# Optimization experiments

Hardware: AMD Instinct MI355X
Metric: run time of the kernel (lower is better)

Reference implementation:

```python
import jax, jax.numpy as jnp
from jax import lax
import numpy as np

# ---- init hyperparameters (from init_kwargs) ----
STRIDE = 1
DP_CHANNELS = 1
ATOM_R = 8
ATOM_C = 8
NUMB_ATOM = 128
T_SC = 3
K = 256
BATCH = 32
IMG = 64


def setup_inputs() -> dict:
    key = jax.random.key(0)
    k1, k2 = jax.random.split(key)
    Y = jax.random.normal(k1, (BATCH, DP_CHANNELS, IMG, IMG), dtype=jnp.float32)
    # ConvTranspose2d weight layout: (numb_atom, dp_channels, atom_c, atom_r)
    W = jax.random.normal(k2, (NUMB_ATOM, DP_CHANNELS, ATOM_C, ATOM_R), dtype=jnp.float32)
    # normalise_weights(): each (i, j) filter divided by its L2 norm
    W = W / jnp.sqrt(jnp.sum(W ** 2, axis=(2, 3), keepdims=True))
    return {"Y": Y, "W_D": W}


def _conv_D(X, W):
    # PyTorch ConvTranspose2d (stride=1, no padding): full convolution with
    # spatially-flipped kernel; W is (in=numb_atom, out=dp_channels, kh, kw).
    kh, kw = W.shape[2], W.shape[3]
    return lax.conv_general_dilated(
        X, jnp.flip(W, (2, 3)), (1, 1),
        [(kh - 1, kh - 1), (kw - 1, kw - 1)],
        dimension_numbers=('NCHW', 'IOHW', 'NCHW'))


def _conv_Dt(R, Wt):
    # PyTorch Conv2d (VALID, stride=1): Wt is (out=numb_atom, in=dp, kh, kw)
    return lax.conv_general_dilated(
        R, Wt, (1, 1), 'VALID', dimension_numbers=('NCHW', 'OIHW', 'NCHW'))


def _hard_threshold_k(X, k):
    # keep the k largest-|.| entries per sample (over flattened C,H,W)
    B = X.shape[0]
    flat = X.reshape(B, -1)
    _, idx = lax.top_k(jnp.abs(flat), k)                      # [B, k]
    vals = jnp.take_along_axis(flat, idx, axis=1)             # [B, k]
    out = jnp.zeros_like(flat).at[jnp.arange(B)[:, None], idx].set(vals)
    return out.reshape(X.shape)


def _linesearch(Y, X, W, Wt, k):
    R = Y - _conv_D(X, W)
    g = _conv_Dt(R, Wt)
    l2_start = jnp.sum(R ** 2)

    def attempt(alpha):
        Xu = _hard_threshold_k(X + alpha * g, k)
        err = jnp.sum((Y - _conv_D(Xu, W)) ** 2)
        return Xu, err

    Xu0, err0 = attempt(jnp.float32(1.0))

    def cond(s):
        _, _, err, count = s
        return (err >= l2_start) & (count <= 15)

    def body(s):
        alpha, _, _, count = s
        alpha = alpha * jnp.float32(0.5)
        Xu, err = attempt(alpha)
        return (alpha, Xu, err, count + 1)

    alpha, Xu, err, _ = lax.while_loop(
        cond, body, (jnp.float32(1.0), Xu0, err0, jnp.int32(0)))
    return Xu, err, alpha


def reference(Y, W_D):
    # D_trans.weight = D.weight.permute(0,1,3,2) -> (numb_atom, dp, atom_r, atom_c)
    Wt = jnp.swapaxes(W_D, 2, 3)
    kh, kw = Wt.shape[2], Wt.shape[3]
    B, _, H, W_sp = Y.shape
    X = jnp.zeros((B, W_D.shape[0], H - kh + 1, W_sp - kw + 1), dtype=Y.dtype)
    for _ in range(T_SC):
        X, _, _ = _linesearch(Y, X, W_D, Wt, K)
    return X
```

## Files before the change

### kernel.cpp

```cpp
#include <hip/hip_runtime.h>
#include <stdint.h>

#define NB   32
#define NCH  128
#define IMG  64
#define IMG2 4096
#define OH   57
#define OHW  3249
#define CHW  415872
#define KTOP 256
#define NATT 17
#define NS   32
#define SCAP 512
#define NCAP 1536
#define NBUCK 8192
#define HSHIFT 18
#define TGT  512
#define RSTRIDE 72
#define NZB  257
#define BMW  12996

typedef unsigned long long ull;

__global__ void k_init(int* support_cnt) {
    if (threadIdx.x < NB) support_cnt[threadIdx.x] = 0;
}

__global__ __launch_bounds__(256) void k_resid(
    const float* __restrict__ Y, const float* __restrict__ W,
    const double* __restrict__ l2prev, const double* __restrict__ errv,
    const uint32_t* __restrict__ sel_idx, const float* __restrict__ sel_val, int t,
    int* __restrict__ support_cnt, ull* __restrict__ sup_iv,
    float* __restrict__ Rg, double* __restrict__ l2cur,
    uint32_t* __restrict__ hist, int* __restrict__ zero_arena)
{
    int bx = blockIdx.x, tid = threadIdx.x;
    if (bx >= NB) {
        int zb = bx - NB;
        if (zb < 256) {
            ((uint4*)hist)[zb * 256 + tid] = make_uint4(0u, 0u, 0u, 0u);
        } else {
            ((uint4*)zero_arena)[tid] = make_uint4(0u, 0u, 0u, 0u);
            ((uint4*)zero_arena)[tid + 256] = make_uint4(0u, 0u, 0u, 0u);
        }
        return;
    }
    int b = bx;
    __shared__ float Rs[IMG2];
    __shared__ uint32_t s_si[KTOP];
    __shared__ float s_sv[KTOP];
    __shared__ double red[256];
    __shared__ int a_sh;

    const float4* Y4 = (const float4*)(Y + b * IMG2);
    float4* R4 = (float4*)Rs;
    for (int i = tid; i < IMG2 / 4; i += 256) R4[i] = Y4[i];

    int n = 0;
    if (t > 0) {
        if (tid < NATT) {
            double e = 0.0;
#pragma unroll 8
            for (int b2 = 0; b2 < NB; ++b2) e += errv[tid * NB + b2];
            red[tid] = e;
        } else if (tid == NATT) {
            double l2 = 0.0;
#pragma unroll 8
            for (int b2 = 0; b2 < NB; ++b2) l2 += l2prev[b2];
            red[NATT] = l2;
        }
        __syncthreads();
        if (tid == 0) {
            double l2 = red[NATT];
            int sel = NATT - 1;
            for (int a2 = 0; a2 < NATT; ++a2) if (red[a2] < l2) { sel = a2; break; }
            a_sh = sel;
        }
        __syncthreads();
        int a = a_sh;
        size_t o = ((size_t)a * NB + b) * KTOP;
        uint32_t mi = sel_idx[o + tid];
        float mv = sel_val[o + tid];
        s_si[tid] = mi;
        s_sv[tid] = mv;
        sup_iv[b * KTOP + tid] = (ull)mi | ((ull)__float_as_uint(mv) << 32);
        if (tid == 0) support_cnt[b] = KTOP;
        n = KTOP;
    }
    __syncthreads();

    for (int task = tid; task < n * 64; task += 256) {
        int i = task >> 6, tap = task & 63, p = tap >> 3, q = tap & 7;
        uint32_t idx = s_si[i];
        float val = s_sv[i];
        int c = idx / OHW, rem = idx % OHW, s = rem / OH, tt = rem % OH;
        float w = W[c * 64 + p * 8 + q];
        atomicAdd(&Rs[(s + p) * IMG + (tt + q)], -val * w);
    }
    __syncthreads();
    double acc = 0.0;
    for (int i = tid; i < IMG2; i += 256) {
        float v = Rs[i];
        Rg[b * IMG2 + i] = v;
        acc += (double)v * (double)v;
    }
    red[tid] = acc; __syncthreads();
    for (int s2 = 128; s2 > 0; s2 >>= 1) { if (tid < s2) red[tid] += red[tid + s2]; __syncthreads(); }
    if (tid == 0) l2cur[b] = red[0];
}

__global__ __launch_bounds__(256) void k_conv(
    const float* __restrict__ Rg, const float* __restrict__ W,
    float* __restrict__ g_out, uint32_t* __restrict__ hist,
    int* __restrict__ done_cnt, uint32_t* __restrict__ thr)
{
    int b = blockIdx.x, cg0 = blockIdx.y, tid = threadIdx.x;
    __shared__ float Rs[71 * 72];
    __shared__ uint32_t hl[NBUCK];
    __shared__ int elect_sh;
    for (int i = tid; i < 71 * 72; i += 256) Rs[i] = 0.f;
    for (int i = tid; i < NBUCK; i += 256) hl[i] = 0u;
    __syncthreads();
    const float4* R4 = (const float4*)(Rg + b * IMG2);
    for (int i = tid; i < 1024; i += 256) {
        int row = i >> 4, col4 = (i & 15) * 4;
        *(float4*)&Rs[row * 72 + col4] = R4[i];
    }
    __syncthreads();
    int csub = tid >> 7;
    int tile = tid & 127;
    bool active = tile < 120;
    int tr = active ? tile / 15 : 0;
    int tc = active ? tile % 15 : 0;
    int s0 = tr * 8, t0 = tc * 4;

    for (int sub = 0; sub < 4; ++sub) {
        int c = cg0 * 8 + sub * 2 + csub;
        int c_s = __builtin_amdgcn_readfirstlane(c);
        const float* Wc = W + c_s * 64;

        float acc[8][4];
#pragma unroll
        for (int r = 0; r < 8; ++r)
#pragma unroll
            for (int cc = 0; cc < 4; ++cc) acc[r][cc] = 0.f;

#pragma unroll
        for (int rho = 0; rho < 15; ++rho) {
            float rb[12];
            const float* rp = &Rs[(s0 + rho) * 72 + t0];
            *(float4*)&rb[0] = *(const float4*)rp;
            *(float4*)&rb[4] = *(const float4*)(rp + 4);
            *(float4*)&rb[8] = *(const float4*)(rp + 8);
#pragma unroll
            for (int r = 0; r < 8; ++r) {
                const int p = rho - r;
                if (p >= 0 && p < 8) {
#pragma unroll
                    for (int q = 0; q < 8; ++q) {
                        float wv = Wc[q * 8 + p];
#pragma unroll
                        for (int cc = 0; cc < 4; ++cc)
                            acc[r][cc] = fmaf(rb[cc + q], wv, acc[r][cc]);
                    }
                }
            }
        }
        if (active) {
            float* go = g_out + (size_t)(b * NCH + c) * OHW;
#pragma unroll
            for (int r = 0; r < 8; ++r) {
                int s = s0 + r;
                if (s < OH) {
#pragma unroll
                    for (int cc = 0; cc < 4; ++cc) {
                        int t = t0 + cc;
                        if (t < OH) {
                            float v = acc[r][cc];
                            go[s * OH + t] = v;
                            uint32_t bits = __float_as_uint(v) & 0x7fffffffu;
                            atomicAdd(&hl[bits >> HSHIFT], 1u);
                        }
                    }
                }
            }
        }
    }
    __syncthreads();
    for (int i = tid; i < NBUCK; i += 256) {
        uint32_t v = hl[i];
        if (v) atomicAdd(&hist[b * NBUCK + i], v);
    }
    __syncthreads();
    if (tid == 0) {
        __threadfence();
        int old = atomicAdd(&done_cnt[b], 1);
        elect_sh = (old == 15) ? 1 : 0;
    }
    __syncthreads();
    if (elect_sh) {
        uint32_t h[32];
        uint32_t s = 0;
        const uint32_t* hb = hist + b * NBUCK + tid * 32;
#pragma unroll
        for (int k = 0; k < 32; ++k) {
            h[k] = __hip_atomic_load(&hb[k], __ATOMIC_RELAXED, __HIP_MEMORY_SCOPE_AGENT);
            s += h[k];
        }
        uint32_t* buf0 = hl;
        uint32_t* buf1 = hl + 256;
        int cur = 0;
        buf0[tid] = s;
        __syncthreads();
        for (int d = 1; d < 256; d <<= 1) {
            uint32_t* bc = cur ? buf1 : buf0;
            uint32_t* bn = cur ? buf0 : buf1;
            uint32_t v = bc[tid];
            if (tid + d < 256) v += bc[tid + d];
            bn[tid] = v;
            cur ^= 1;
            __syncthreads();
        }
        uint32_t* bc = cur ? buf1 : buf0;
        uint32_t sufme = bc[tid];
        uint32_t base  = (tid < 255) ? bc[tid + 1] : 0u;
        if (tid == 0 && bc[0] < TGT) thr[b] = 0u;
        if (base < TGT && sufme >= TGT) {
            uint32_t acc2 = base; int bk = 0;
#pragma unroll
            for (int k = 31; k >= 0; --k) {
                acc2 += h[k];
                if (acc2 >= TGT) { bk = tid * 32 + k; break; }
            }
            thr[b] = (uint32_t)bk << HSHIFT;
        }
    }
}

__global__ __launch_bounds__(256) void k_collect(
    const float* __restrict__ g, const uint32_t* __restrict__ thr,
    int* __restrict__ cand_cnt, uint32_t* __restrict__ cand_idx, float* __restrict__ cand_g)
{
    int b = blockIdx.y;
    int i4 = blockIdx.x * 256 + threadIdx.x;
    if (i4 >= CHW / 4) return;
    int slice = blockIdx.x & (NS - 1);
    uint32_t tb = thr[b];
    float4 v4 = ((const float4*)(g + (size_t)b * CHW))[i4];
    float vv[4] = { v4.x, v4.y, v4.z, v4.w };
#pragma unroll
    for (int k = 0; k < 4; ++k) {
        uint32_t bits = __float_as_uint(vv[k]) & 0x7fffffffu;
        if (bits >= tb) {
            int pos = atomicAdd(&cand_cnt[b * NS + slice], 1);
            if (pos < SCAP) {
                cand_idx[(b * NS + slice) * SCAP + pos] = (uint32_t)(i4 * 4 + k);
                cand_g[(b * NS + slice) * SCAP + pos] = vv[k];
            }
        }
    }
}

__global__ __launch_bounds__(1024) void k_suppg(
    const float* __restrict__ g,
    const int* __restrict__ support_cnt, const ull* __restrict__ sup_iv,
    const int* __restrict__ cand_cnt, const uint32_t* __restrict__ cand_idx,
    const float* __restrict__ cand_g,
    uint4* __restrict__ ns_pack, ull* __restrict__ sup_gp, ull* __restrict__ kb_all)
{
    int b = blockIdx.x, tid = threadIdx.x, lane = tid & 63;
    __shared__ uint32_t bm[BMW];
    __shared__ int cnts[NS];
    __shared__ ull ck[NCAP];
    __shared__ float cg_l[NCAP];
    __shared__ int nns_sh;
    int n = support_cnt[b];
    for (int i = tid; i < BMW / 4; i += 1024) ((uint4*)bm)[i] = make_uint4(0u, 0u, 0u, 0u);
    if (tid < NS) cnts[tid] = min(cand_cnt[b * NS + tid], SCAP);
    if (tid == 0) nns_sh = 0;
    __syncthreads();
    if (tid < KTOP) {
        float gv = 0.f, vs = 0.f;
        uint32_t nidx;
        if (tid < n) {
            ull iv = sup_iv[b * KTOP + tid];
            uint32_t idx = (uint32_t)iv;
            nidx = idx;
            vs = __uint_as_float((uint32_t)(iv >> 32));
            atomicOr(&bm[idx >> 5], 1u << (idx & 31));
            gv = g[(size_t)b * CHW + idx];
            int c = idx / OHW, r = idx % OHW, s = r / OH, t = r % OH;
            uint32_t pk = (uint32_t)((c << 12) | (s << 6) | t);
            sup_gp[b * KTOP + tid] = ((ull)__float_as_uint(gv) << 32) | (ull)pk;
        } else {
            nidx = (uint32_t)(CHW + tid);
            sup_gp[b * KTOP + tid] = 0ull;
        }
        ull klo = (ull)(uint32_t)(~nidx);
#pragma unroll
        for (int a2 = 0; a2 < NATT; ++a2) {
            float v2 = (tid < n) ? fmaf(ldexpf(1.f, -a2), gv, vs) : 0.f;
            kb_all[((size_t)a2 * NB + b) * KTOP + tid] =
                ((ull)(__float_as_uint(v2) & 0x7fffffffu) << 32) | klo;
        }
    }
    __syncthreads();
    for (int t0 = tid; t0 < NS * SCAP; t0 += 1024) {
        int s = t0 >> 9, j = t0 & (SCAP - 1);
        bool keep = false; uint32_t idx = 0; float gv = 0.f;
        if (j < cnts[s]) {
            idx = cand_idx[(b * NS + s) * SCAP + j];
            gv = cand_g[(b * NS + s) * SCAP + j];
            keep = ((bm[idx >> 5] >> (idx & 31)) & 1u) == 0u;
        }
        ull mk = __ballot(keep);
        if (mk) {
            int basep = 0;
            if (lane == 0) basep = atomicAdd(&nns_sh, (int)__popcll(mk));
            basep = __shfl(basep, 0, 64);
            if (keep) {
                int p = basep + (int)__popcll(mk & ((1ull << lane) - 1ull));
                if (p < NCAP) {
                    ck[p] = ((ull)(__float_as_uint(gv) & 0x7fffffffu) << 32) | (ull)(uint32_t)(~idx);
                    cg_l[p] = gv;
                }
            }
        }
    }
    __syncthreads();
    int nns = min(nns_sh, NCAP);
    int nns8 = (nns + 7) & ~7;
    for (int i = nns + tid; i < nns8; i += 1024) ck[i] = 0ull;
    __syncthreads();
    ull myk[2]; int myr[2];
#pragma unroll
    for (int q = 0; q < 2; ++q) { int i = tid + 1024 * q; myk[q] = (i < nns) ? ck[i] : 0ull; myr[q] = 0; }
    for (int j = 0; j < nns8; j += 8) {
        ull t0 = ck[j], t1 = ck[j+1], t2 = ck[j+2], t3 = ck[j+3];
        ull t4 = ck[j+4], t5 = ck[j+5], t6 = ck[j+6], t7 = ck[j+7];
#pragma unroll
        for (int q = 0; q < 2; ++q) {
            myr[q] += ((t0 > myk[q]) ? 1 : 0) + ((t1 > myk[q]) ? 1 : 0)
                    + ((t2 > myk[q]) ? 1 : 0) + ((t3 > myk[q]) ? 1 : 0)
                    + ((t4 > myk[q]) ? 1 : 0) + ((t5 > myk[q]) ? 1 : 0)
                    + ((t6 > myk[q]) ? 1 : 0) + ((t7 > myk[q]) ? 1 : 0);
        }
    }
#pragma unroll
    for (int q = 0; q < 2; ++q) {
        int i = tid + 1024 * q;
        if (i < nns && myr[q] < KTOP) {
            uint32_t idx = ~(uint32_t)myk[q];
            int r = myr[q];
            int c = idx / OHW, rr = idx % OHW, s = rr / OH, t = rr % OH;
            uint32_t pk = (uint32_t)((c << 12) | (s << 6) | t);
            ns_pack[b * KTOP + r] = make_uint4(idx, __float_as_uint(cg_l[i]), pk, 0u);
        }
    }
}

__global__ __launch_bounds__(512) void k_att2(
    const float* __restrict__ Y, const float* __restrict__ W,
    const int* __restrict__ support_cnt, const ull* __restrict__ sup_iv,
    const ull* __restrict__ sup_gp, const uint4* __restrict__ ns_pack,
    const ull* __restrict__ kb_all,
    uint32_t* __restrict__ sel_idx, float* __restrict__ sel_val, double* __restrict__ err)
{
    int a = blockIdx.x, b = blockIdx.y, tid = threadIdx.x;
    int lane = tid & 63, wid = tid >> 6;
    float alpha = ldexpf(1.f, -a);
    int n = support_cnt[b];

    __shared__ float recon[64 * RSTRIDE];
    __shared__ ull kA[KTOP];
    __shared__ ull s_pv[KTOP];
    __shared__ uint32_t s_idx[KTOP];
    __shared__ double redd[8];

    uint32_t myi = 0, mypk = 0;
    float myv = 0.f;
    ull myk = 0;
    if (tid < KTOP) {
        uint4 np = ns_pack[b * KTOP + tid];
        myi = np.x;
        myv = alpha * __uint_as_float(np.y);
        mypk = np.z;
        myk = ((ull)(__float_as_uint(myv) & 0x7fffffffu) << 32) | (ull)(uint32_t)(~myi);
        kA[tid] = myk;
    } else {
        int t2 = tid - KTOP;
        ull gp = sup_gp[b * KTOP + t2];
        ull iv = sup_iv[b * KTOP + t2];
        if (t2 < n) {
            myi = (uint32_t)iv;
            myv = fmaf(alpha, __uint_as_float((uint32_t)(gp >> 32)),
                       __uint_as_float((uint32_t)(iv >> 32)));
            mypk = (uint32_t)gp;
        } else {
            myi = (uint32_t)(CHW + t2);
            myv = 0.f; mypk = 0u;
        }
        myk = ((ull)(__float_as_uint(myv) & 0x7fffffffu) << 32) | (ull)(uint32_t)(~myi);
    }

    const float4* Y4 = (const float4*)(Y + b * IMG2);
    float4 y0 = Y4[tid * 2], y1 = Y4[tid * 2 + 1];

    for (int i = tid; i < 64 * RSTRIDE; i += 512) recon[i] = 0.f;
    __syncthreads();

    const ull* __restrict__ kb = kb_all + ((size_t)a * NB + b) * KTOP;
    int cb0 = 0, cb1 = 0;
    for (int j = 0; j < KTOP; j += 8) {
        ull t0 = kb[j],     t1 = kb[j + 1], t2 = kb[j + 2], t3 = kb[j + 3];
        ull t4 = kb[j + 4], t5 = kb[j + 5], t6 = kb[j + 6], t7 = kb[j + 7];
        cb0 += ((t0 > myk) ? 1 : 0) + ((t1 > myk) ? 1 : 0)
             + ((t2 > myk) ? 1 : 0) + ((t3 > myk) ? 1 : 0);
        cb1 += ((t4 > myk) ? 1 : 0) + ((t5 > myk) ? 1 : 0)
             + ((t6 > myk) ? 1 : 0) + ((t7 > myk) ? 1 : 0);
    }
    int cb = cb0 + cb1;
    int rank;
    if (tid < KTOP) {
        rank = tid + cb;
    } else {
        int lo = 0, hi = KTOP;
        while (lo < hi) { int mid = (lo + hi) >> 1; if (kA[mid] > myk) lo = mid + 1; else hi = mid; }
        rank = lo + cb;
    }
    if (rank < KTOP) {
        s_pv[rank] = ((ull)__float_as_uint(myv) << 32) | (ull)mypk;
        s_idx[rank] = myi;
    }
    __syncthreads();

    {
        int p = lane >> 3, q = lane & 7;
        ull pv[4]; float wv[4];
#pragma unroll
        for (int j = 0; j < 4; ++j) pv[j] = s_pv[wid + 8 * j];
#pragma unroll
        for (int j = 0; j < 4; ++j) wv[j] = W[(((uint32_t)pv[j]) >> 12) * 64 + lane];
#pragma unroll
        for (int k4 = 0; k4 < 32; k4 += 4) {
            ull npv[4] = {0, 0, 0, 0}; float nwv[4] = {0.f, 0.f, 0.f, 0.f};
            if (k4 + 4 < 32) {
#pragma unroll
                for (int j = 0; j < 4; ++j) npv[j] = s_pv[wid + 8 * (k4 + 4 + j)];
#pragma unroll
                for (int j = 0; j < 4; ++j) nwv[j] = W[(((uint32_t)npv[j]) >> 12) * 64 + lane];
            }
#pragma unroll
            for (int j = 0; j < 4; ++j) {
                uint32_t pk = (uint32_t)pv[j];
                float val = __uint_as_float((uint32_t)(pv[j] >> 32));
                int s = (pk >> 6) & 63, t = pk & 63;
                atomicAdd(&recon[(s + p) * RSTRIDE + (t + q)], val * wv[j]);
            }
#pragma unroll
            for (int j = 0; j < 4; ++j) { pv[j] = npv[j]; wv[j] = nwv[j]; }
        }
    }
    __syncthreads();

    double accd = 0.0;
    {
        int idx0 = tid * 2;
        const float* rr = &recon[(idx0 >> 4) * RSTRIDE + (idx0 & 15) * 4];
        float d0 = y0.x - rr[0]; accd += (double)d0 * (double)d0;
        float d1 = y0.y - rr[1]; accd += (double)d1 * (double)d1;
        float d2 = y0.z - rr[2]; accd += (double)d2 * (double)d2;
        float d3 = y0.w - rr[3]; accd += (double)d3 * (double)d3;
        int idx1 = tid * 2 + 1;
        rr = &recon[(idx1 >> 4) * RSTRIDE + (idx1 & 15) * 4];
        float e0 = y1.x - rr[0]; accd += (double)e0 * (double)e0;
        float e1 = y1.y - rr[1]; accd += (double)e1 * (double)e1;
        float e2 = y1.z - rr[2]; accd += (double)e2 * (double)e2;
        float e3 = y1.w - rr[3]; accd += (double)e3 * (double)e3;
    }
    for (int d = 32; d > 0; d >>= 1) accd += __shfl_xor(accd, d, 64);
    if (lane == 0) redd[wid] = accd;
    __syncthreads();
    if (tid == 0) {
        double e = 0.0;
#pragma unroll
        for (int w2 = 0; w2 < 8; ++w2) e += redd[w2];
        err[a * NB + b] = e;
    }

    if (tid < KTOP) {
        size_t o = ((size_t)a * NB + b) * KTOP;
        ull pvt = s_pv[tid];
        sel_idx[o + tid] = s_idx[tid];
        sel_val[o + tid] = __uint_as_float((uint32_t)(pvt >> 32));
    }
}

__global__ void k_outzero(float4* __restrict__ out) {
    int i = blockIdx.x * 256 + threadIdx.x;
    if (i < (NB * CHW) / 4) out[i] = make_float4(0.f, 0.f, 0.f, 0.f);
}

__global__ __launch_bounds__(256) void k_scatter2(
    const double* __restrict__ l2f, const double* __restrict__ errv,
    const uint32_t* __restrict__ sel_idx, const float* __restrict__ sel_val,
    float* __restrict__ out)
{
    int b = blockIdx.x, tid = threadIdx.x;
    __shared__ double red2[NATT + 1];
    __shared__ int a_sh;
    if (tid < NATT) {
        double e = 0.0;
#pragma unroll 8
        for (int b2 = 0; b2 < NB; ++b2) e += errv[tid * NB + b2];
        red2[tid] = e;
    } else if (tid == NATT) {
        double l2 = 0.0;
#pragma unroll 8
        for (int b2 = 0; b2 < NB; ++b2) l2 += l2f[b2];
        red2[NATT] = l2;
    }
    __syncthreads();
    if (tid == 0) {
        double l2 = red2[NATT];
        int sel = NATT - 1;
        for (int a2 = 0; a2 < NATT; ++a2) if (red2[a2] < l2) { sel = a2; break; }
        a_sh = sel;
    }
    __syncthreads();
    size_t o = ((size_t)a_sh * NB + b) * KTOP;
    out[(size_t)b * CHW + sel_idx[o + tid]] = sel_val[o + tid];
}

static size_t align256(size_t x) { return (x + 255) & ~(size_t)255; }

extern "C" void kernel_launch(void* const* d_in, const int* in_sizes, int n_in,
                              void* d_out, int out_size, void* d_ws, size_t ws_size,
                              hipStream_t stream)
{
    const float* Y = (const float*)d_in[0];
    const float* W = (const float*)d_in[1];
    float* out = (float*)d_out;

    char* p = (char*)d_ws;
    size_t off = 0;
    auto carve = [&](size_t bytes) { void* r = p + off; off = align256(off + bytes); return r; };
    float*    Rg          = (float*)   carve(NB * IMG2 * sizeof(float));
    uint32_t* hist        = (uint32_t*)carve((size_t)NB * NBUCK * sizeof(uint32_t));
    uint32_t* thr         = (uint32_t*)carve(NB * sizeof(uint32_t));
    int*      zero_arena  = (int*)     carve(8192 * sizeof(int));
    double*   l2part      = (double*)  carve(2 * NB * sizeof(double));
    double*   err         = (double*)  carve((size_t)NATT * NB * sizeof(double));
    int*      support_cnt = (int*)     carve(NB * sizeof(int));
    ull*      sup_iv      = (ull*)     carve((size_t)NB * KTOP * sizeof(ull));
    uint32_t* sel_idx     = (uint32_t*)carve((size_t)NATT * NB * KTOP * sizeof(uint32_t));
    float*    sel_val     = (float*)   carve((size_t)NATT * NB * KTOP * sizeof(float));
    uint32_t* cand_idx    = (uint32_t*)carve((size_t)NB * NS * SCAP * sizeof(uint32_t));
    float*    cand_g      = (float*)   carve((size_t)NB * NS * SCAP * sizeof(float));
    uint4*    ns_pack     = (uint4*)   carve((size_t)NB * KTOP * sizeof(uint4));
    ull*      sup_gp      = (ull*)     carve((size_t)NB * KTOP * sizeof(ull));
    ull*      kb_all      = (ull*)     carve((size_t)NATT * NB * KTOP * sizeof(ull));
    (void)ws_size; (void)in_sizes; (void)n_in; (void)out_size;

    int*      cand_cnt    = zero_arena;
    int*      done_cnt    = zero_arena + 1024;

    k_init<<<1, 64, 0, stream>>>(support_cnt);
    for (int t = 0; t < 3; ++t) {
        double* l2cur  = l2part + (t & 1) * NB;
        double* l2prev = l2part + ((t + 1) & 1) * NB;
        k_resid<<<NB + NZB, 256, 0, stream>>>(Y, W, l2prev, err, sel_idx, sel_val, t,
                                              support_cnt, sup_iv, Rg, l2cur, hist, zero_arena);
        k_conv<<<dim3(NB, 16), 256, 0, stream>>>(Rg, W, out, hist, done_cnt, thr);
        k_collect<<<dim3((CHW / 4 + 255) / 256, NB), 256, 0, stream>>>(out, thr, cand_cnt, cand_idx, cand_g);
        k_suppg<<<NB, 1024, 0, stream>>>(out, support_cnt, sup_iv,
                                         cand_cnt, cand_idx, cand_g,
                                         ns_pack, sup_gp, kb_all);
        k_att2<<<dim3(NATT, NB), 512, 0, stream>>>(Y, W, support_cnt, sup_iv,
                                                   sup_gp, ns_pack, kb_all,
                                                   sel_idx, sel_val, err);
    }
    k_outzero<<<((NB * CHW) / 4 + 255) / 256, 256, 0, stream>>>((float4*)out);
    k_scatter2<<<NB, 256, 0, stream>>>(l2part, err, sel_idx, sel_val, out);
}
```

Baseline: 699.2 us.

## Split histogram threshold into own kernel and fold output zeroing into k_att2

The last-block-elected threshold scan at the end of k_conv, with its done-counter atomics and fence, moves into a separate small k_thresh kernel launched after k_conv. The standalone k_outzero kernel is removed. The final iteration's k_att2 blocks now zero the output buffer with a grid-stride loop after their main work. The aim is to drop the fence and atomic election from every conv block and save one launch for zeroing, at the cost of an extra launch for the threshold and extra tail work in k_att2.

```diff
diff --git a/kernel.cpp b/kernel.cpp
--- a/kernel.cpp
+++ b/kernel.cpp
@@ -32,7 +32,7 @@
     const uint32_t* __restrict__ sel_idx, const float* __restrict__ sel_val, int t,
     int* __restrict__ support_cnt, ull* __restrict__ sup_iv,
     float* __restrict__ Rg, double* __restrict__ l2cur,
-    uint32_t* __restrict__ hist, int* __restrict__ zero_arena)
+    uint32_t* __restrict__ hist, int* __restrict__ cand_cnt)
 {
     int bx = blockIdx.x, tid = threadIdx.x;
     if (bx >= NB) {
@@ -40,8 +40,7 @@
         if (zb < 256) {
             ((uint4*)hist)[zb * 256 + tid] = make_uint4(0u, 0u, 0u, 0u);
         } else {
-            ((uint4*)zero_arena)[tid] = make_uint4(0u, 0u, 0u, 0u);
-            ((uint4*)zero_arena)[tid + 256] = make_uint4(0u, 0u, 0u, 0u);
+            ((uint4*)cand_cnt)[tid] = make_uint4(0u, 0u, 0u, 0u);
         }
         return;
     }
@@ -111,13 +110,11 @@
 
 __global__ __launch_bounds__(256) void k_conv(
     const float* __restrict__ Rg, const float* __restrict__ W,
-    float* __restrict__ g_out, uint32_t* __restrict__ hist,
-    int* __restrict__ done_cnt, uint32_t* __restrict__ thr)
+    float* __restrict__ g_out, uint32_t* __restrict__ hist)
 {
     int b = blockIdx.x, cg0 = blockIdx.y, tid = threadIdx.x;
     __shared__ float Rs[71 * 72];
     __shared__ uint32_t hl[NBUCK];
-    __shared__ int elect_sh;
     for (int i = tid; i < 71 * 72; i += 256) Rs[i] = 0.f;
     for (int i = tid; i < NBUCK; i += 256) hl[i] = 0u;
     __syncthreads();
@@ -174,10 +171,10 @@
                 if (s < OH) {
 #pragma unroll
                     for (int cc = 0; cc < 4; ++cc) {
-                        int t = t0 + cc;
-                        if (t < OH) {
+                        int tcol = t0 + cc;
+                        if (tcol < OH) {
                             float v = acc[r][cc];
-                            go[s * OH + t] = v;
+                            go[s * OH + tcol] = v;
                             uint32_t bits = __float_as_uint(v) & 0x7fffffffu;
                             atomicAdd(&hl[bits >> HSHIFT], 1u);
                         }
@@ -191,49 +188,38 @@
         uint32_t v = hl[i];
         if (v) atomicAdd(&hist[b * NBUCK + i], v);
     }
-    __syncthreads();
-    if (tid == 0) {
-        __threadfence();
-        int old = atomicAdd(&done_cnt[b], 1);
-        elect_sh = (old == 15) ? 1 : 0;
-    }
-    __syncthreads();
-    if (elect_sh) {
-        uint32_t h[32];
-        uint32_t s = 0;
-        const uint32_t* hb = hist + b * NBUCK + tid * 32;
-#pragma unroll
-        for (int k = 0; k < 32; ++k) {
-            h[k] = __hip_atomic_load(&hb[k], __ATOMIC_RELAXED, __HIP_MEMORY_SCOPE_AGENT);
-            s += h[k];
-        }
-        uint32_t* buf0 = hl;
-        uint32_t* buf1 = hl + 256;
-        int cur = 0;
-        buf0[tid] = s;
+}
+
+__global__ __launch_bounds__(256) void k_thresh(const uint32_t* __restrict__ hist,
+                                                uint32_t* __restrict__ thr) {
+    int b = blockIdx.x, tid = threadIdx.x;
+    uint32_t h[32];
+    uint32_t s = 0;
+    const uint32_t* hb = hist + b * NBUCK + tid * 32;
+#pragma unroll
+    for (int k = 0; k < 32; ++k) { h[k] = hb[k]; s += h[k]; }
+    __shared__ uint32_t buf[2][256];
+    int cur = 0;
+    buf[0][tid] = s;
+    __syncthreads();
+    for (int d = 1; d < 256; d <<= 1) {
+        uint32_t v = buf[cur][tid];
+        if (tid + d < 256) v += buf[cur][tid + d];
+        buf[cur ^ 1][tid] = v;
+        cur ^= 1;
         __syncthreads();
-        for (int d = 1; d < 256; d <<= 1) {
-            uint32_t* bc = cur ? buf1 : buf0;
-            uint32_t* bn = cur ? buf0 : buf1;
-            uint32_t v = bc[tid];
-            if (tid + d < 256) v += bc[tid + d];
-            bn[tid] = v;
-            cur ^= 1;
-            __syncthreads();
-        }
-        uint32_t* bc = cur ? buf1 : buf0;
-        uint32_t sufme = bc[tid];
-        uint32_t base  = (tid < 255) ? bc[tid + 1] : 0u;
-        if (tid == 0 && bc[0] < TGT) thr[b] = 0u;
-        if (base < TGT && sufme >= TGT) {
-            uint32_t acc2 = base; int bk = 0;
-#pragma unroll
-            for (int k = 31; k >= 0; --k) {
-                acc2 += h[k];
-                if (acc2 >= TGT) { bk = tid * 32 + k; break; }
-            }
-            thr[b] = (uint32_t)bk << HSHIFT;
-        }
+    }
+    uint32_t sufme = buf[cur][tid];
+    uint32_t base  = (tid < 255) ? buf[cur][tid + 1] : 0u;
+    if (tid == 0 && buf[cur][0] < TGT) thr[b] = 0u;
+    if (base < TGT && sufme >= TGT) {
+        uint32_t acc = base; int bk = 0;
+#pragma unroll
+        for (int k = 31; k >= 0; --k) {
+            acc += h[k];
+            if (acc >= TGT) { bk = tid * 32 + k; break; }
+        }
+        thr[b] = (uint32_t)bk << HSHIFT;
     }
 }
 
@@ -364,7 +350,8 @@
     const int* __restrict__ support_cnt, const ull* __restrict__ sup_iv,
     const ull* __restrict__ sup_gp, const uint4* __restrict__ ns_pack,
     const ull* __restrict__ kb_all,
-    uint32_t* __restrict__ sel_idx, float* __restrict__ sel_val, double* __restrict__ err)
+    uint32_t* __restrict__ sel_idx, float* __restrict__ sel_val, double* __restrict__ err,
+    float* __restrict__ outz, int zf)
 {
     int a = blockIdx.x, b = blockIdx.y, tid = threadIdx.x;
     int lane = tid & 63, wid = tid >> 6;
@@ -494,11 +481,13 @@
         sel_idx[o + tid] = s_idx[tid];
         sel_val[o + tid] = __uint_as_float((uint32_t)(pvt >> 32));
     }
-}
-
-__global__ void k_outzero(float4* __restrict__ out) {
-    int i = blockIdx.x * 256 + threadIdx.x;
-    if (i < (NB * CHW) / 4) out[i] = make_float4(0.f, 0.f, 0.f, 0.f);
+
+    if (zf) {
+        float4* o4 = (float4*)outz;
+        size_t fb = (size_t)a * NB + b;
+        for (size_t i = fb * 512 + tid; i < (size_t)NB * CHW / 4; i += (size_t)NATT * NB * 512)
+            o4[i] = make_float4(0.f, 0.f, 0.f, 0.f);
+    }
 }
 
 __global__ __launch_bounds__(256) void k_scatter2(
@@ -548,7 +537,7 @@
     float*    Rg          = (float*)   carve(NB * IMG2 * sizeof(float));
     uint32_t* hist        = (uint32_t*)carve((size_t)NB * NBUCK * sizeof(uint32_t));
     uint32_t* thr         = (uint32_t*)carve(NB * sizeof(uint32_t));
-    int*      zero_arena  = (int*)     carve(8192 * sizeof(int));
+    int*      cand_cnt    = (int*)     carve(NB * NS * sizeof(int));
     double*   l2part      = (double*)  carve(2 * NB * sizeof(double));
     double*   err         = (double*)  carve((size_t)NATT * NB * sizeof(double));
     int*      support_cnt = (int*)     carve(NB * sizeof(int));
@@ -562,24 +551,22 @@
     ull*      kb_all      = (ull*)     carve((size_t)NATT * NB * KTOP * sizeof(ull));
     (void)ws_size; (void)in_sizes; (void)n_in; (void)out_size;
 
-    int*      cand_cnt    = zero_arena;
-    int*      done_cnt    = zero_arena + 1024;
-
     k_init<<<1, 64, 0, stream>>>(support_cnt);
     for (int t = 0; t < 3; ++t) {
         double* l2cur  = l2part + (t & 1) * NB;
         double* l2prev = l2part + ((t + 1) & 1) * NB;
         k_resid<<<NB + NZB, 256, 0, stream>>>(Y, W, l2prev, err, sel_idx, sel_val, t,
-                                              support_cnt, sup_iv, Rg, l2cur, hist, zero_arena);
-        k_conv<<<dim3(NB, 16), 256, 0, stream>>>(Rg, W, out, hist, done_cnt, thr);
+                                              support_cnt, sup_iv, Rg, l2cur, hist, cand_cnt);
+        k_conv<<<dim3(NB, 16), 256, 0, stream>>>(Rg, W, out, hist);
+        k_thresh<<<NB, 256, 0, stream>>>(hist, thr);
         k_collect<<<dim3((CHW / 4 + 255) / 256, NB), 256, 0, stream>>>(out, thr, cand_cnt, cand_idx, cand_g);
         k_suppg<<<NB, 1024, 0, stream>>>(out, support_cnt, sup_iv,
                                          cand_cnt, cand_idx, cand_g,
                                          ns_pack, sup_gp, kb_all);
         k_att2<<<dim3(NATT, NB), 512, 0, stream>>>(Y, W, support_cnt, sup_iv,
                                                    sup_gp, ns_pack, kb_all,
-                                                   sel_idx, sel_val, err);
-    }
-    k_outzero<<<((NB * CHW) / 4 + 255) / 256, 256, 0, stream>>>((float4*)out);
+                                                   sel_idx, sel_val, err,
+                                                   out, (t == 2) ? 1 : 0);
+    }
     k_scatter2<<<NB, 256, 0, stream>>>(l2part, err, sel_idx, sel_val, out);
 }
```

Result: faster. 642.4 us (-8.1%).
